# Kernel tuning notes

Measured on AMD Instinct MI355X. Metric: run time of the kernel, lower is better.

## Reference

```python
import jax, jax.numpy as jnp
import numpy as np

NEG_SLOPE = 0.01  # torch leaky_relu default

def _leaky_relu(x):
    return jnp.where(x >= 0, x, NEG_SLOPE * x)

def setup_inputs() -> dict:
    key = jax.random.key(0)
    ks = jax.random.split(key, 12)
    n_drug, n_disease, n_edges, d = 10000, 10000, 1000000, 100
    inp = {
        "x_drug": jax.random.normal(ks[0], (n_drug, d), dtype=jnp.float32),
        "x_disease": jax.random.normal(ks[1], (n_disease, d), dtype=jnp.float32),
        "edge_label_index": jax.random.randint(ks[2], (2, n_edges), 0, n_drug, dtype=jnp.int64),
        "W1": jax.random.normal(ks[3], (200, 128), dtype=jnp.float32) * 0.07,
        "b1": jax.random.normal(ks[4], (128,), dtype=jnp.float32) * 0.01,
        "W2": jax.random.normal(ks[5], (128, 32), dtype=jnp.float32) * 0.09,
        "b2": jax.random.normal(ks[6], (32,), dtype=jnp.float32) * 0.01,
        "W3": jax.random.normal(ks[7], (32, 16), dtype=jnp.float32) * 0.18,
        "b3": jax.random.normal(ks[8], (16,), dtype=jnp.float32) * 0.01,
        "W4": jax.random.normal(ks[9], (16, 1), dtype=jnp.float32) * 0.25,
        "b4": jax.random.normal(ks[10], (1,), dtype=jnp.float32) * 0.01,
    }
    return inp

def reference(x_drug, x_disease, edge_label_index, W1, b1, W2, b2, W3, b3, W4, b4):
    # gather per-edge node embeddings and concat -> [E, 200]
    ef = jnp.concatenate([x_drug[edge_label_index[0]],
                          x_disease[edge_label_index[1]]], axis=-1)
    ef = _leaky_relu(ef @ W1 + b1)
    ef = _leaky_relu(ef @ W2 + b2)
    ef = _leaky_relu(ef @ W3 + b3)
    ef = ef @ W4 + b4
    return jnp.squeeze(ef, axis=-1)
```

## Files before the change

### kernel.cpp

```cpp
#include <hip/hip_runtime.h>
#include <cstdint>
#include <cstddef>

typedef _Float16 hf2   __attribute__((ext_vector_type(2)));
typedef _Float16 f16x8 __attribute__((ext_vector_type(8)));
typedef float    f32x4 __attribute__((ext_vector_type(4)));

__device__ __forceinline__ f16x8 q2h8(uint4 q) { union { uint4 q; f16x8 h; } c; c.q = q; return c.h; }
__device__ __forceinline__ hf2 pkrtz(float lo, float hi) {
    auto v = __builtin_amdgcn_cvt_pkrtz(lo, hi);
    union { decltype(v) a; hf2 b; } c; c.a = v; return c.b;
}
__device__ __forceinline__ float lreluf(float x) { return fmaxf(x, 0.01f * x); }
__device__ __forceinline__ f16x8 lrelu8(uint4 a, uint4 b) {
    f16x8 s = q2h8(a) + q2h8(b);
    f16x8 m = s * (_Float16)0.01f;
    return __builtin_elementwise_max(s, m);
}

__global__ __launch_bounds__(256) void node_proj2(
    const float* __restrict__ xd, const float* __restrict__ xi,
    const float* __restrict__ W1, const float* __restrict__ b1,
    _Float16* __restrict__ Pd, _Float16* __restrict__ Pi,
    int nd, int ni, int nblk_d, int nblk_i,
    const float* __restrict__ W2, const float* __restrict__ W3,
    _Float16* __restrict__ W2f, _Float16* __restrict__ W3f,
    const unsigned* __restrict__ ew, long long nwords, int* __restrict__ flag)
{
    const int t = threadIdx.x;
    const int nproj = nblk_d + nblk_i;

    if ((int)blockIdx.x >= nproj) {
        if ((int)blockIdx.x == nproj) {
            for (int idx = t; idx < 4096; idx += 256) {
                int i  = idx & 7;
                int l  = (idx >> 3) & 63;
                int kt = (idx >> 9) & 3;
                int nt = (idx >> 11) & 1;
                int k = kt * 32 + 8 * (l >> 4) + i;
                int j = nt * 16 + (l & 15);
                W2f[idx] = (_Float16)W2[k * 32 + j];
            }
            for (int idx = t; idx < 512; idx += 256) {
                int i = idx & 7, l = idx >> 3;
                W3f[idx] = (_Float16)W3[(8 * (l >> 4) + i) * 16 + (l & 15)];
            }
        } else if (t < 64) {
            const long long pairs = nwords / 2;
            const long long step  = pairs / 64;
            unsigned v = 0;
            for (int s = 0; s < 4; ++s) {
                long long p = (long long)t * step + (long long)s * (step / 4 + 1);
                if (p < pairs) v |= ew[2 * p + 1];
            }
            unsigned long long ball = __ballot(v != 0);
            if (t == 0) *flag = (ball == 0ULL) ? 1 : 0;
        }
        return;
    }

    __shared__ float xs[1600];
    const int c  = t & 127;
    const int ty = t >> 7;
    const bool dis = (int)blockIdx.x >= nblk_d;
    const int b = dis ? (blockIdx.x - nblk_d) : blockIdx.x;
    const int n = dis ? ni : nd;
    const float* x = dis ? xi : xd;
    const float* W = dis ? (W1 + 100 * 128) : W1;
    _Float16* P = dis ? Pi : Pd;
    const float bv = dis ? b1[c] : 0.f;
    const int r0 = b * 16;

    const long long gbase = (long long)r0 * 100;
    const long long lim   = (long long)n * 100;
    for (int idx = t; idx < 1600; idx += 256) {
        long long g = gbase + idx;
        xs[idx] = (g < lim) ? x[g] : 0.f;
    }
    __syncthreads();

    float acc[8];
#pragma unroll
    for (int i = 0; i < 8; ++i) acc[i] = bv;

    const float4* xs4 = (const float4*)xs;
#pragma unroll 5
    for (int kk = 0; kk < 25; ++kk) {
        float w0 = W[(4 * kk + 0) * 128 + c];
        float w1 = W[(4 * kk + 1) * 128 + c];
        float w2 = W[(4 * kk + 2) * 128 + c];
        float w3 = W[(4 * kk + 3) * 128 + c];
#pragma unroll
        for (int i = 0; i < 8; ++i) {
            float4 xv = xs4[(ty * 8 + i) * 25 + kk];
            acc[i] = fmaf(xv.x, w0, acc[i]);
            acc[i] = fmaf(xv.y, w1, acc[i]);
            acc[i] = fmaf(xv.z, w2, acc[i]);
            acc[i] = fmaf(xv.w, w3, acc[i]);
        }
    }
#pragma unroll
    for (int i = 0; i < 8; ++i) {
        int r = r0 + ty * 8 + i;
        if (r < n) P[(size_t)r * 128 + c] = (_Float16)acc[i];
    }
}

__global__ __launch_bounds__(256, 4) void edge_mlp(
    const void* __restrict__ eidx_raw,
    const _Float16* __restrict__ Pd, const _Float16* __restrict__ Pi,
    const _Float16* __restrict__ W2f, const float* __restrict__ b2,
    const _Float16* __restrict__ W3f, const float* __restrict__ b3,
    const float* __restrict__ W4, const float* __restrict__ b4,
    const int* __restrict__ flag64,
    float* __restrict__ out, int E)
{
    __shared__ __align__(16) _Float16 H2[4][64 * 40];

    const int t  = threadIdx.x;
    const int l  = t & 63;
    const int w  = t >> 6;
    const int er = l & 15;
    const int cg = l >> 4;
    const int base = blockIdx.x * 256 + w * 64;
    const int e_c = min(base + l, E - 1);
    _Float16* Hw = H2[w];

    int i0, i1;
    if (*flag64) {
        const long long* p = (const long long*)eidx_raw;
        i0 = (int)p[e_c];
        i1 = (int)p[(size_t)E + e_c];
    } else {
        const int* p = (const int*)eidx_raw;
        i0 = p[e_c];
        i1 = p[(size_t)E + e_c];
    }

    int j0[4], j1[4];
#pragma unroll
    for (int q = 0; q < 4; ++q) {
        j0[q] = __shfl(i0, q * 16 + er, 64);
        j1[q] = __shfl(i1, q * 16 + er, 64);
    }

    f16x8 bf0[4], bf1[4];
    {
        const uint4* W2q = (const uint4*)W2f;
#pragma unroll
        for (int kt = 0; kt < 4; ++kt) {
            bf0[kt] = q2h8(W2q[kt * 64 + l]);
            bf1[kt] = q2h8(W2q[256 + kt * 64 + l]);
        }
    }
    const float b2v0 = b2[er], b2v1 = b2[16 + er];

    uint4 dA[2][4], dB[2][4];
    {
        const uint4* rD = (const uint4*)(Pd + (size_t)j0[0] * 128);
        const uint4* rI = (const uint4*)(Pi + (size_t)j1[0] * 128);
#pragma unroll
        for (int kt = 0; kt < 4; ++kt) {
            dA[0][kt] = rD[kt * 4 + cg];
            dB[0][kt] = rI[kt * 4 + cg];
        }
    }

#pragma unroll
    for (int q = 0; q < 4; ++q) {
        if (q < 3) {
            const uint4* rD = (const uint4*)(Pd + (size_t)j0[q + 1] * 128);
            const uint4* rI = (const uint4*)(Pi + (size_t)j1[q + 1] * 128);
#pragma unroll
            for (int kt = 0; kt < 4; ++kt) {
                dA[(q + 1) & 1][kt] = rD[kt * 4 + cg];
                dB[(q + 1) & 1][kt] = rI[kt * 4 + cg];
            }
        }

        f32x4 c0 = {0.f, 0.f, 0.f, 0.f}, c1 = {0.f, 0.f, 0.f, 0.f};
#pragma unroll
        for (int kt = 0; kt < 4; ++kt) {
            f16x8 af = lrelu8(dA[q & 1][kt], dB[q & 1][kt]);
            c0 = __builtin_amdgcn_mfma_f32_16x16x32_f16(af, bf0[kt], c0, 0, 0, 0);
            c1 = __builtin_amdgcn_mfma_f32_16x16x32_f16(af, bf1[kt], c1, 0, 0, 0);
        }

#pragma unroll
        for (int r = 0; r < 4; ++r) {
            const int e = q * 16 + 4 * cg + r;
            Hw[e * 40 + er]      = (_Float16)lreluf(c0[r] + b2v0);
            Hw[e * 40 + 16 + er] = (_Float16)lreluf(c1[r] + b2v1);
        }
    }

    const f16x8 w3f = q2h8(((const uint4*)W3f)[l]);
    const float4 b3q = ((const float4*)b3)[cg];
    const float4 w4q = ((const float4*)W4)[cg];
    const float  b4v = b4[0];

#pragma unroll
    for (int q = 0; q < 4; ++q) {
        const int e2 = q * 16 + er;
        f16x8 hv = *(const f16x8*)&Hw[e2 * 40 + 8 * cg];

        f32x4 d3 = __builtin_amdgcn_mfma_f32_16x16x32_f16(
            w3f, hv, (f32x4){0.f, 0.f, 0.f, 0.f}, 0, 0, 0);

        float v = lreluf(d3[0] + b3q.x) * w4q.x;
        v      += lreluf(d3[1] + b3q.y) * w4q.y;
        v      += lreluf(d3[2] + b3q.z) * w4q.z;
        v      += lreluf(d3[3] + b3q.w) * w4q.w;
        v += __shfl_xor(v, 16, 64);
        v += __shfl_xor(v, 32, 64);

        if (cg == 0) {
            const int eo = base + q * 16 + er;
            if (eo < E) out[eo] = v + b4v;
        }
    }
}

extern "C" void kernel_launch(void* const* d_in, const int* in_sizes, int n_in,
                              void* d_out, int out_size, void* d_ws, size_t ws_size,
                              hipStream_t stream)
{
    const float* x_drug = (const float*)d_in[0];
    const float* x_dis  = (const float*)d_in[1];
    const void*  eidx   = d_in[2];
    const float* W1 = (const float*)d_in[3];
    const float* b1 = (const float*)d_in[4];
    const float* W2 = (const float*)d_in[5];
    const float* b2 = (const float*)d_in[6];
    const float* W3 = (const float*)d_in[7];
    const float* b3 = (const float*)d_in[8];
    const float* W4 = (const float*)d_in[9];
    const float* b4 = (const float*)d_in[10];

    const int nd = in_sizes[0] / 100;
    const int ni = in_sizes[1] / 100;
    const int E  = in_sizes[2] / 2;

    char* ws = (char*)d_ws;
    _Float16* Pd  = (_Float16*)ws;                   size_t off = (size_t)nd * 128 * 2;
    _Float16* Pi  = (_Float16*)(ws + off);           off += (size_t)ni * 128 * 2;
    _Float16* W2f = (_Float16*)(ws + off);           off += 4096 * 2;
    _Float16* W3f = (_Float16*)(ws + off);           off += 512 * 2;
    int* flag = (int*)(ws + off);

    const int nblk_d = (nd + 15) / 16;
    const int nblk_i = (ni + 15) / 16;

    node_proj2<<<nblk_d + nblk_i + 2, 256, 0, stream>>>(
        x_drug, x_dis, W1, b1, Pd, Pi, nd, ni, nblk_d, nblk_i,
        W2, W3, W2f, W3f,
        (const unsigned*)eidx, 2LL * E, flag);

    edge_mlp<<<(E + 255) / 256, 256, 0, stream>>>(eidx, Pd, Pi,
                                                  W2f, b2, W3f, b3, W4, b4,
                                                  flag, (float*)d_out, E);
}
```

Before: 161.2 us.

## Stage W2/W3 in LDS and hand-schedule gather loads with inline asm vmcnt

The edge MLP kernel now copies the packed W2/W3 fp16 weights into shared memory once per block and reads MFMA B operands from LDS instead of keeping them in registers. The per-edge-row gathers use inline-asm global_load_dwordx4 with explicit vmcnt waits, keeping two quads of gathers in flight while the previous quad is consumed. The index load becomes branchless, and the occupancy hint drops from 4 to 3 waves per SIMD. The aim is deeper memory-level parallelism on the random gathers, at the cost of an extra block-wide sync, LDS traffic for weights, and lower occupancy.

```diff
diff --git a/kernel.cpp b/kernel.cpp
--- a/kernel.cpp
+++ b/kernel.cpp
@@ -5,18 +5,22 @@
 typedef _Float16 hf2   __attribute__((ext_vector_type(2)));
 typedef _Float16 f16x8 __attribute__((ext_vector_type(8)));
 typedef float    f32x4 __attribute__((ext_vector_type(4)));
-
-__device__ __forceinline__ f16x8 q2h8(uint4 q) { union { uint4 q; f16x8 h; } c; c.q = q; return c.h; }
-__device__ __forceinline__ hf2 pkrtz(float lo, float hi) {
-    auto v = __builtin_amdgcn_cvt_pkrtz(lo, hi);
-    union { decltype(v) a; hf2 b; } c; c.a = v; return c.b;
-}
+typedef unsigned int u32x4 __attribute__((ext_vector_type(4)));
+
+__device__ __forceinline__ f16x8 b2h8(u32x4 q) { union { u32x4 q; f16x8 h; } c; c.q = q; return c.h; }
 __device__ __forceinline__ float lreluf(float x) { return fmaxf(x, 0.01f * x); }
-__device__ __forceinline__ f16x8 lrelu8(uint4 a, uint4 b) {
-    f16x8 s = q2h8(a) + q2h8(b);
+__device__ __forceinline__ f16x8 lrelu8(u32x4 a, u32x4 b) {
+    f16x8 s = b2h8(a) + b2h8(b);
     f16x8 m = s * (_Float16)0.01f;
     return __builtin_elementwise_max(s, m);
 }
+
+#define GLOAD(dst, ptr, off) \
+    asm volatile("global_load_dwordx4 %0, %1, off offset:" #off \
+                 : "=v"(dst) : "v"(ptr) : "memory")
+#define VMCNT(n) do { \
+    asm volatile("s_waitcnt vmcnt(" #n ")" ::: "memory"); \
+    __builtin_amdgcn_sched_barrier(0); } while (0)
 
 __global__ __launch_bounds__(256) void node_proj2(
     const float* __restrict__ xd, const float* __restrict__ xi,
@@ -106,16 +110,17 @@
     }
 }
 
-__global__ __launch_bounds__(256, 4) void edge_mlp(
+__global__ __launch_bounds__(256, 3) void edge_mlp(
     const void* __restrict__ eidx_raw,
     const _Float16* __restrict__ Pd, const _Float16* __restrict__ Pi,
     const _Float16* __restrict__ W2f, const float* __restrict__ b2,
-    const _Float16* __restrict__ W3f, const float* __restrict__ b3,
+    const float* __restrict__ b3,
     const float* __restrict__ W4, const float* __restrict__ b4,
     const int* __restrict__ flag64,
     float* __restrict__ out, int E)
 {
-    __shared__ __align__(16) _Float16 H2[4][64 * 40];
+    __shared__ __align__(16) u32x4    Ws[576];
+    __shared__ __align__(16) _Float16 H2s[4][64 * 40];
 
     const int t  = threadIdx.x;
     const int l  = t & 63;
@@ -123,19 +128,20 @@
     const int er = l & 15;
     const int cg = l >> 4;
     const int base = blockIdx.x * 256 + w * 64;
+    _Float16* Hw = H2s[w];
+
+    const int f = *flag64;
+
+    {
+        const u32x4* src = (const u32x4*)W2f;
+        for (int idx = t; idx < 576; idx += 256) Ws[idx] = src[idx];
+    }
+    __syncthreads();
+
     const int e_c = min(base + l, E - 1);
-    _Float16* Hw = H2[w];
-
-    int i0, i1;
-    if (*flag64) {
-        const long long* p = (const long long*)eidx_raw;
-        i0 = (int)p[e_c];
-        i1 = (int)p[(size_t)E + e_c];
-    } else {
-        const int* p = (const int*)eidx_raw;
-        i0 = p[e_c];
-        i1 = p[(size_t)E + e_c];
-    }
+    const char* pb = (const char*)eidx_raw;
+    const int i0 = *(const int*)(pb + (f ? 8 * (size_t)e_c : 4 * (size_t)e_c));
+    const int i1 = *(const int*)(pb + (f ? 8 * ((size_t)E + e_c) : 4 * ((size_t)E + e_c)));
 
     int j0[4], j1[4];
 #pragma unroll
@@ -143,58 +149,63 @@
         j0[q] = __shfl(i0, q * 16 + er, 64);
         j1[q] = __shfl(i1, q * 16 + er, 64);
     }
-
-    f16x8 bf0[4], bf1[4];
-    {
-        const uint4* W2q = (const uint4*)W2f;
-#pragma unroll
-        for (int kt = 0; kt < 4; ++kt) {
-            bf0[kt] = q2h8(W2q[kt * 64 + l]);
-            bf1[kt] = q2h8(W2q[256 + kt * 64 + l]);
-        }
-    }
+    const char* pD0 = (const char*)(Pd + (size_t)j0[0] * 128) + cg * 16;
+    const char* pI0 = (const char*)(Pi + (size_t)j1[0] * 128) + cg * 16;
+    const char* pD1 = (const char*)(Pd + (size_t)j0[1] * 128) + cg * 16;
+    const char* pI1 = (const char*)(Pi + (size_t)j1[1] * 128) + cg * 16;
+    const char* pD2 = (const char*)(Pd + (size_t)j0[2] * 128) + cg * 16;
+    const char* pI2 = (const char*)(Pi + (size_t)j1[2] * 128) + cg * 16;
+    const char* pD3 = (const char*)(Pd + (size_t)j0[3] * 128) + cg * 16;
+    const char* pI3 = (const char*)(Pi + (size_t)j1[3] * 128) + cg * 16;
+
     const float b2v0 = b2[er], b2v1 = b2[16 + er];
 
-    uint4 dA[2][4], dB[2][4];
-    {
-        const uint4* rD = (const uint4*)(Pd + (size_t)j0[0] * 128);
-        const uint4* rI = (const uint4*)(Pi + (size_t)j1[0] * 128);
-#pragma unroll
-        for (int kt = 0; kt < 4; ++kt) {
-            dA[0][kt] = rD[kt * 4 + cg];
-            dB[0][kt] = rI[kt * 4 + cg];
-        }
-    }
-
-#pragma unroll
-    for (int q = 0; q < 4; ++q) {
-        if (q < 3) {
-            const uint4* rD = (const uint4*)(Pd + (size_t)j0[q + 1] * 128);
-            const uint4* rI = (const uint4*)(Pi + (size_t)j1[q + 1] * 128);
-#pragma unroll
-            for (int kt = 0; kt < 4; ++kt) {
-                dA[(q + 1) & 1][kt] = rD[kt * 4 + cg];
-                dB[(q + 1) & 1][kt] = rI[kt * 4 + cg];
-            }
-        }
-
-        f32x4 c0 = {0.f, 0.f, 0.f, 0.f}, c1 = {0.f, 0.f, 0.f, 0.f};
-#pragma unroll
-        for (int kt = 0; kt < 4; ++kt) {
-            f16x8 af = lrelu8(dA[q & 1][kt], dB[q & 1][kt]);
-            c0 = __builtin_amdgcn_mfma_f32_16x16x32_f16(af, bf0[kt], c0, 0, 0, 0);
-            c1 = __builtin_amdgcn_mfma_f32_16x16x32_f16(af, bf1[kt], c1, 0, 0, 0);
-        }
-
-#pragma unroll
-        for (int r = 0; r < 4; ++r) {
-            const int e = q * 16 + 4 * cg + r;
-            Hw[e * 40 + er]      = (_Float16)lreluf(c0[r] + b2v0);
-            Hw[e * 40 + 16 + er] = (_Float16)lreluf(c1[r] + b2v1);
-        }
-    }
-
-    const f16x8 w3f = q2h8(((const uint4*)W3f)[l]);
+#define ISSUE(A, V, pD, pI) do { \
+    GLOAD(A##0, pD, 0); GLOAD(A##1, pD, 64); GLOAD(A##2, pD, 128); GLOAD(A##3, pD, 192); \
+    GLOAD(V##0, pI, 0); GLOAD(V##1, pI, 64); GLOAD(V##2, pI, 128); GLOAD(V##3, pI, 192); } while (0)
+
+#define CONSUME(q, A, V) do { \
+    f32x4 c0 = {0.f,0.f,0.f,0.f}, c1 = {0.f,0.f,0.f,0.f}; \
+    f16x8 af; \
+    af = lrelu8(A##0, V##0); \
+    c0 = __builtin_amdgcn_mfma_f32_16x16x32_f16(af, b2h8(Ws[0 * 64 + l]), c0, 0, 0, 0); \
+    c1 = __builtin_amdgcn_mfma_f32_16x16x32_f16(af, b2h8(Ws[256 + 0 * 64 + l]), c1, 0, 0, 0); \
+    af = lrelu8(A##1, V##1); \
+    c0 = __builtin_amdgcn_mfma_f32_16x16x32_f16(af, b2h8(Ws[1 * 64 + l]), c0, 0, 0, 0); \
+    c1 = __builtin_amdgcn_mfma_f32_16x16x32_f16(af, b2h8(Ws[256 + 1 * 64 + l]), c1, 0, 0, 0); \
+    af = lrelu8(A##2, V##2); \
+    c0 = __builtin_amdgcn_mfma_f32_16x16x32_f16(af, b2h8(Ws[2 * 64 + l]), c0, 0, 0, 0); \
+    c1 = __builtin_amdgcn_mfma_f32_16x16x32_f16(af, b2h8(Ws[256 + 2 * 64 + l]), c1, 0, 0, 0); \
+    af = lrelu8(A##3, V##3); \
+    c0 = __builtin_amdgcn_mfma_f32_16x16x32_f16(af, b2h8(Ws[3 * 64 + l]), c0, 0, 0, 0); \
+    c1 = __builtin_amdgcn_mfma_f32_16x16x32_f16(af, b2h8(Ws[256 + 3 * 64 + l]), c1, 0, 0, 0); \
+    _Pragma("unroll") \
+    for (int r = 0; r < 4; ++r) { \
+        const int e = (q) * 16 + 4 * cg + r; \
+        Hw[e * 40 + er]      = (_Float16)lreluf(c0[r] + b2v0); \
+        Hw[e * 40 + 16 + er] = (_Float16)lreluf(c1[r] + b2v1); \
+    } } while (0)
+
+    u32x4 A00, A01, A02, A03, V00, V01, V02, V03;
+    u32x4 A10, A11, A12, A13, V10, V11, V12, V13;
+
+    ISSUE(A0, V0, pD0, pI0);
+    ISSUE(A1, V1, pD1, pI1);
+    VMCNT(8);
+    CONSUME(0, A0, V0);
+    ISSUE(A0, V0, pD2, pI2);
+    VMCNT(8);
+    CONSUME(1, A1, V1);
+    ISSUE(A1, V1, pD3, pI3);
+    VMCNT(8);
+    CONSUME(2, A0, V0);
+    VMCNT(0);
+    CONSUME(3, A1, V1);
+
+#undef ISSUE
+#undef CONSUME
+
+    const f16x8 w3f = b2h8(Ws[512 + l]);
     const float4 b3q = ((const float4*)b3)[cg];
     const float4 w4q = ((const float4*)W4)[cg];
     const float  b4v = b4[0];
@@ -203,7 +214,6 @@
     for (int q = 0; q < 4; ++q) {
         const int e2 = q * 16 + er;
         f16x8 hv = *(const f16x8*)&Hw[e2 * 40 + 8 * cg];
-
         f32x4 d3 = __builtin_amdgcn_mfma_f32_16x16x32_f16(
             w3f, hv, (f32x4){0.f, 0.f, 0.f, 0.f}, 0, 0, 0);
 
@@ -257,6 +267,6 @@
         (const unsigned*)eidx, 2LL * E, flag);
 
     edge_mlp<<<(E + 255) / 256, 256, 0, stream>>>(eidx, Pd, Pi,
-                                                  W2f, b2, W3f, b3, W4, b4,
+                                                  W2f, b2, b3, W4, b4,
                                                   flag, (float*)d_out, E);
 }
```

New measurement: 160.2 us. No clear change (-0.6%).
